# Performance work log

Measured on AMD Instinct MI355X. Metric: run time of the kernel, lower is better.

Reference implementation:

```python
import jax, jax.numpy as jnp
import numpy as np

# Static SMPL kinematic tree (24 joints)
PARENTS = [-1, 0, 0, 0, 1, 2, 3, 4, 5, 6, 7, 8, 9, 9, 9, 12, 13, 14, 16, 17, 18, 19, 20, 21]
NJ = 24      # num joints
FS = 6       # local_feature_size
NF = 7       # bone_dim (1) + FS


def _topo_order(parents):
    children = {i: [] for i in range(len(parents))}
    roots = []
    for i, p in enumerate(parents):
        (roots if p == -1 else children[p]).append(i)
    order = []
    queue = roots[:]
    while queue:
        c = queue.pop(0)
        order.append(c)
        queue.extend(sorted(children[c]))
    return order

TOPO = _topo_order(PARENTS)


def setup_inputs() -> dict:
    key = jax.random.key(0)
    ks = jax.random.split(key, 5)
    B = 524288
    x = jax.random.normal(ks[0], (B, NJ, 1), dtype=jnp.float32)
    s = 1.0 / np.sqrt(NF)
    # Stacked per-joint weights. For the root joint, the parent-feature rows of
    # W1 are multiplied by a zero virtual parent feature, which is exactly
    # equivalent to the original Linear(1, 7) root MLP.
    W1 = jax.random.uniform(ks[1], (NJ, NF, NF), jnp.float32, -s, s)
    b1 = jax.random.uniform(ks[2], (NJ, NF), jnp.float32, -s, s)
    W2 = jax.random.uniform(ks[3], (NJ, NF, FS), jnp.float32, -s, s)
    b2 = jax.random.uniform(ks[4], (NJ, FS), jnp.float32, -s, s)
    return {"x": x, "W1": W1, "b1": b1, "W2": W2, "b2": b2}


def reference(x, W1, b1, W2, b2):
    # x: [B, NJ, 1]; sequential propagation over the fixed kinematic tree.
    B = x.shape[0]
    feats = [None] * NJ
    zero_pf = jnp.zeros((B, FS), x.dtype)
    for i in TOPO:
        p = PARENTS[i]
        pf = zero_pf if p == -1 else feats[p]
        inp = jnp.concatenate([x[:, i, :], pf], axis=-1)  # [B, 7]
        h = jax.nn.relu(inp @ W1[i] + b1[i])               # [B, 7]
        feats[i] = jax.nn.relu(h @ W2[i] + b2[i])          # [B, 6]
    return jnp.concatenate(feats, axis=-1)                 # [B, 144]
```

## Files before the change

### kernel.cpp

```cpp
#include <hip/hip_runtime.h>

#define NJ 24
#define NF 7
#define FS 6
#define THREADS 256
#define CUNITS 12
#define PAD 13

typedef float v4f __attribute__((ext_vector_type(4)));

__device__ constexpr int kParents[NJ] = {-1, 0, 0, 0, 1, 2, 3, 4, 5, 6, 7, 8,
                                          9, 9, 9, 12, 13, 14, 16, 17, 18, 19, 20, 21};

#define JOINT(i)                                                              \
    {                                                                         \
        const int p_ = kParents[i];                                           \
        float inp_[NF];                                                       \
        inp_[0] = xr[i];                                                      \
        _Pragma("unroll")                                                     \
        for (int j = 0; j < FS; ++j)                                          \
            inp_[1 + j] = (p_ < 0) ? 0.0f : feats[(p_ < 0) ? 0 : p_][j];      \
        float h_[NF];                                                         \
        _Pragma("unroll")                                                     \
        for (int j = 0; j < NF; ++j) h_[j] = b1[(i) * NF + j];                \
        _Pragma("unroll")                                                     \
        for (int k = 0; k < NF; ++k) {                                        \
            const float a_ = inp_[k];                                         \
            _Pragma("unroll")                                                 \
            for (int j = 0; j < NF; ++j)                                      \
                h_[j] = fmaf(a_, W1[(i) * NF * NF + k * NF + j], h_[j]);      \
        }                                                                     \
        _Pragma("unroll")                                                     \
        for (int j = 0; j < NF; ++j) h_[j] = fmaxf(h_[j], 0.0f);              \
        float f_[FS];                                                         \
        _Pragma("unroll")                                                     \
        for (int j = 0; j < FS; ++j) f_[j] = b2[(i) * FS + j];                \
        _Pragma("unroll")                                                     \
        for (int k = 0; k < NF; ++k) {                                        \
            const float a_ = h_[k];                                           \
            _Pragma("unroll")                                                 \
            for (int j = 0; j < FS; ++j)                                      \
                f_[j] = fmaf(a_, W2[(i) * NF * FS + k * FS + j], f_[j]);      \
        }                                                                     \
        _Pragma("unroll")                                                     \
        for (int j = 0; j < FS; ++j) {                                        \
            f_[j] = fmaxf(f_[j], 0.0f);                                       \
            feats[i][j] = f_[j];                                              \
        }                                                                     \
        if ((i) & 1) {                                                        \
            const int pp_ = ((i) >> 1) & 3;                                   \
            v4f* st_ = myStage + pp_ * 3;                                     \
            st_[0] = (v4f){feats[(i) - 1][0], feats[(i) - 1][1],              \
                           feats[(i) - 1][2], feats[(i) - 1][3]};             \
            st_[1] = (v4f){feats[(i) - 1][4], feats[(i) - 1][5],              \
                           f_[0], f_[1]};                                     \
            st_[2] = (v4f){f_[2], f_[3], f_[4], f_[5]};                       \
        }                                                                     \
    }

#define FLUSH(C)                                                              \
    {                                                                         \
        _Pragma("unroll")                                                     \
        for (int j = 0; j < CUNITS; ++j) {                                    \
            const int G = j * 64 + lane;                                      \
            const int s = G / CUNITS;                                         \
            const int q = G - s * CUNITS;                                     \
            fr[j] = sm[wid][s * PAD + q];                                     \
        }                                                                     \
        _Pragma("unroll")                                                     \
        for (int j = 0; j < CUNITS; ++j) {                                    \
            v4f* dst_ = reinterpret_cast<v4f*>(                               \
                reinterpret_cast<char*>(obase) + voff[j] + (C) * 192);        \
            __builtin_nontemporal_store(fr[j], dst_);                         \
        }                                                                     \
    }

#define KEEP12(A)                                                             \
    asm volatile("" :: "v"(A[0]), "v"(A[1]), "v"(A[2]), "v"(A[3]),            \
                 "v"(A[4]), "v"(A[5]), "v"(A[6]), "v"(A[7]),                  \
                 "v"(A[8]), "v"(A[9]), "v"(A[10]), "v"(A[11]));

__global__ __launch_bounds__(THREADS, 3) void se1d_kernel(
    const float* __restrict__ x,
    const float* __restrict__ W1,
    const float* __restrict__ b1,
    const float* __restrict__ W2,
    const float* __restrict__ b2,
    float* __restrict__ out, int B)
{
    __shared__ v4f sm[THREADS / 64][64 * PAD];

    const int t    = threadIdx.x;
    const int lane = t & 63;
    const int wid  = __builtin_amdgcn_readfirstlane(threadIdx.x >> 6);
    const int b    = blockIdx.x * THREADS + t;
    const int wb   = blockIdx.x * THREADS + wid * 64;

    v4f* const myStage = &sm[wid][lane * PAD];
    v4f* const obase = reinterpret_cast<v4f*>(out) + (size_t)wb * 36;

    int voff[CUNITS];
    #pragma unroll
    for (int j = 0; j < CUNITS; ++j) {
        const int G = j * 64 + lane;
        const int s = G / CUNITS;
        const int q = G - s * CUNITS;
        voff[j] = (s * 36 + q) * 16;
    }

    float xr[NJ];
    {
        const v4f* xv = reinterpret_cast<const v4f*>(x + (size_t)b * NJ);
        #pragma unroll
        for (int c = 0; c < NJ / 4; ++c) {
            v4f v = __builtin_nontemporal_load(xv + c);
            xr[c * 4 + 0] = v.x; xr[c * 4 + 1] = v.y;
            xr[c * 4 + 2] = v.z; xr[c * 4 + 3] = v.w;
        }
    }

    float feats[NJ][FS];
    v4f fr[CUNITS];

    JOINT(0) JOINT(1) JOINT(2) JOINT(3) JOINT(4) JOINT(5) JOINT(6) JOINT(7)
    FLUSH(0);
    JOINT(8) JOINT(9) JOINT(10) JOINT(11)
    JOINT(12) JOINT(13) JOINT(14) JOINT(15)
    FLUSH(1);
    JOINT(16) JOINT(17) JOINT(18) JOINT(19)
    JOINT(20) JOINT(21) JOINT(22) JOINT(23)
    FLUSH(2);

    KEEP12(fr);
    (void)B;
}

extern "C" void kernel_launch(void* const* d_in, const int* in_sizes, int n_in,
                              void* d_out, int out_size, void* d_ws, size_t ws_size,
                              hipStream_t stream) {
    const float* x  = (const float*)d_in[0];
    const float* W1 = (const float*)d_in[1];
    const float* b1 = (const float*)d_in[2];
    const float* W2 = (const float*)d_in[3];
    const float* b2 = (const float*)d_in[4];
    float* out = (float*)d_out;
    const int B = in_sizes[0] / NJ;
    const int grid = B / THREADS;
    hipLaunchKernelGGL(se1d_kernel, dim3(grid), dim3(THREADS), 0, stream,
                       x, W1, b1, W2, b2, out, B);
}
```

Measured before the change: 92.71 us.

## Stage per-joint weights in LDS with padded vector layout, drop staging pad

Copies all W1/b1/W2/b2 into a padded shared-memory table at block start, so per-joint weights come from LDS as broadcast vector reads instead of scalar global loads. The output staging buffer loses its padding (stride 12 instead of 13), which may bring back LDS bank conflicts. Nontemporal loads and stores become plain ones, store offsets are recomputed inline instead of held in registers, and the occupancy hint drops from 3 to 2. The trade is an extra sync and a larger LDS footprint in exchange for cheaper weight fetches.

```diff
diff --git a/kernel.cpp b/kernel.cpp
--- a/kernel.cpp
+++ b/kernel.cpp
@@ -5,7 +5,7 @@
 #define FS 6
 #define THREADS 256
 #define CUNITS 12
-#define PAD 13
+#define JSTRIDE 128
 
 typedef float v4f __attribute__((ext_vector_type(4)));
 
@@ -21,33 +21,46 @@
         for (int j = 0; j < FS; ++j)                                          \
             inp_[1 + j] = (p_ < 0) ? 0.0f : feats[(p_ < 0) ? 0 : p_][j];      \
         float h_[NF];                                                         \
-        _Pragma("unroll")                                                     \
-        for (int j = 0; j < NF; ++j) h_[j] = b1[(i) * NF + j];                \
+        {                                                                     \
+            const v4f* bb = reinterpret_cast<const v4f*>(&sw[(i) * JSTRIDE + 56]); \
+            v4f u0 = bb[0], u1 = bb[1];                                       \
+            h_[0] = u0.x; h_[1] = u0.y; h_[2] = u0.z; h_[3] = u0.w;           \
+            h_[4] = u1.x; h_[5] = u1.y; h_[6] = u1.z;                         \
+        }                                                                     \
         _Pragma("unroll")                                                     \
         for (int k = 0; k < NF; ++k) {                                        \
             const float a_ = inp_[k];                                         \
-            _Pragma("unroll")                                                 \
-            for (int j = 0; j < NF; ++j)                                      \
-                h_[j] = fmaf(a_, W1[(i) * NF * NF + k * NF + j], h_[j]);      \
+            const v4f* wr = reinterpret_cast<const v4f*>(&sw[(i) * JSTRIDE + k * 8]); \
+            v4f w0 = wr[0], w1 = wr[1];                                       \
+            h_[0] = fmaf(a_, w0.x, h_[0]); h_[1] = fmaf(a_, w0.y, h_[1]);     \
+            h_[2] = fmaf(a_, w0.z, h_[2]); h_[3] = fmaf(a_, w0.w, h_[3]);     \
+            h_[4] = fmaf(a_, w1.x, h_[4]); h_[5] = fmaf(a_, w1.y, h_[5]);     \
+            h_[6] = fmaf(a_, w1.z, h_[6]);                                    \
         }                                                                     \
         _Pragma("unroll")                                                     \
         for (int j = 0; j < NF; ++j) h_[j] = fmaxf(h_[j], 0.0f);              \
         float f_[FS];                                                         \
-        _Pragma("unroll")                                                     \
-        for (int j = 0; j < FS; ++j) f_[j] = b2[(i) * FS + j];                \
+        {                                                                     \
+            const v4f* bb = reinterpret_cast<const v4f*>(&sw[(i) * JSTRIDE + 120]); \
+            v4f u0 = bb[0], u1 = bb[1];                                       \
+            f_[0] = u0.x; f_[1] = u0.y; f_[2] = u0.z; f_[3] = u0.w;           \
+            f_[4] = u1.x; f_[5] = u1.y;                                       \
+        }                                                                     \
         _Pragma("unroll")                                                     \
         for (int k = 0; k < NF; ++k) {                                        \
             const float a_ = h_[k];                                           \
-            _Pragma("unroll")                                                 \
-            for (int j = 0; j < FS; ++j)                                      \
-                f_[j] = fmaf(a_, W2[(i) * NF * FS + k * FS + j], f_[j]);      \
+            const v4f* wr = reinterpret_cast<const v4f*>(&sw[(i) * JSTRIDE + 64 + k * 8]); \
+            v4f w0 = wr[0], w1 = wr[1];                                       \
+            f_[0] = fmaf(a_, w0.x, f_[0]); f_[1] = fmaf(a_, w0.y, f_[1]);     \
+            f_[2] = fmaf(a_, w0.z, f_[2]); f_[3] = fmaf(a_, w0.w, f_[3]);     \
+            f_[4] = fmaf(a_, w1.x, f_[4]); f_[5] = fmaf(a_, w1.y, f_[5]);     \
         }                                                                     \
         _Pragma("unroll")                                                     \
         for (int j = 0; j < FS; ++j) {                                        \
             f_[j] = fmaxf(f_[j], 0.0f);                                       \
             feats[i][j] = f_[j];                                              \
         }                                                                     \
-        if ((i) & 1) {                                                        \
+        if ((i) & 1) {  \
             const int pp_ = ((i) >> 1) & 3;                                   \
             v4f* st_ = myStage + pp_ * 3;                                     \
             st_[0] = (v4f){feats[(i) - 1][0], feats[(i) - 1][1],              \
@@ -65,13 +78,16 @@
             const int G = j * 64 + lane;                                      \
             const int s = G / CUNITS;                                         \
             const int q = G - s * CUNITS;                                     \
-            fr[j] = sm[wid][s * PAD + q];                                     \
+            fr[j] = sm[wid][s * CUNITS + q];                                  \
         }                                                                     \
         _Pragma("unroll")                                                     \
         for (int j = 0; j < CUNITS; ++j) {                                    \
-            v4f* dst_ = reinterpret_cast<v4f*>(                               \
-                reinterpret_cast<char*>(obase) + voff[j] + (C) * 192);        \
-            __builtin_nontemporal_store(fr[j], dst_);                         \
+            const int G = j * 64 + lane;                                      \
+            const int s = G / CUNITS;                                         \
+            const int q = G - s * CUNITS;                                     \
+            *reinterpret_cast<v4f*>(                                          \
+                reinterpret_cast<char*>(obase) +                              \
+                (s * 36 + q) * 16 + (C) * 192) = fr[j];                       \
         }                                                                     \
     }
 
@@ -80,7 +96,7 @@
                  "v"(A[4]), "v"(A[5]), "v"(A[6]), "v"(A[7]),                  \
                  "v"(A[8]), "v"(A[9]), "v"(A[10]), "v"(A[11]));
 
-__global__ __launch_bounds__(THREADS, 3) void se1d_kernel(
+__global__ __launch_bounds__(THREADS, 2) void se1d_kernel(
     const float* __restrict__ x,
     const float* __restrict__ W1,
     const float* __restrict__ b1,
@@ -88,7 +104,8 @@
     const float* __restrict__ b2,
     float* __restrict__ out, int B)
 {
-    __shared__ v4f sm[THREADS / 64][64 * PAD];
+    __shared__ float sw[NJ * JSTRIDE];
+    __shared__ v4f sm[THREADS / 64][64 * CUNITS];
 
     const int t    = threadIdx.x;
     const int lane = t & 63;
@@ -96,28 +113,40 @@
     const int b    = blockIdx.x * THREADS + t;
     const int wb   = blockIdx.x * THREADS + wid * 64;
 
-    v4f* const myStage = &sm[wid][lane * PAD];
+    for (int idx = t; idx < NJ * JSTRIDE; idx += THREADS) {
+        const int jnt = idx >> 7, r = idx & 127;
+        float v = 0.0f;
+        if (r < 56) {
+            const int k = r >> 3, j = r & 7;
+            if (j < NF) v = W1[jnt * NF * NF + k * NF + j];
+        } else if (r < 64) {
+            const int j = r - 56;
+            if (j < NF) v = b1[jnt * NF + j];
+        } else if (r < 120) {
+            const int k = (r - 64) >> 3, j = (r - 64) & 7;
+            if (j < FS) v = W2[jnt * NF * FS + k * FS + j];
+        } else {
+            const int j = r - 120;
+            if (j < FS) v = b2[jnt * FS + j];
+        }
+        sw[idx] = v;
+    }
+
+    v4f* const myStage = &sm[wid][lane * CUNITS];
     v4f* const obase = reinterpret_cast<v4f*>(out) + (size_t)wb * 36;
-
-    int voff[CUNITS];
-    #pragma unroll
-    for (int j = 0; j < CUNITS; ++j) {
-        const int G = j * 64 + lane;
-        const int s = G / CUNITS;
-        const int q = G - s * CUNITS;
-        voff[j] = (s * 36 + q) * 16;
-    }
 
     float xr[NJ];
     {
         const v4f* xv = reinterpret_cast<const v4f*>(x + (size_t)b * NJ);
         #pragma unroll
         for (int c = 0; c < NJ / 4; ++c) {
-            v4f v = __builtin_nontemporal_load(xv + c);
+            v4f v = xv[c];
             xr[c * 4 + 0] = v.x; xr[c * 4 + 1] = v.y;
             xr[c * 4 + 2] = v.z; xr[c * 4 + 3] = v.w;
         }
     }
+
+    __syncthreads();
 
     float feats[NJ][FS];
     v4f fr[CUNITS];
```

Result: slower. 111.1 us (+19.8%).

## Process four batch groups per block with software-prefetched input loads

Applied to the files above, without the earlier changes.

Each block now handles four consecutive 256-row groups in a loop. The next group's x is prefetched into registers while the current group computes, and the launch grid shrinks by four. The aim is to hide input load latency and amortize per-block setup such as the voff computation. Occupancy hint drops from 3 to 2 because the prefetch buffer raises register pressure, which could reduce latency hiding across waves.

```diff
diff --git a/kernel.cpp b/kernel.cpp
--- a/kernel.cpp
+++ b/kernel.cpp
@@ -6,6 +6,7 @@
 #define THREADS 256
 #define CUNITS 12
 #define PAD 13
+#define KGROUPS 4
 
 typedef float v4f __attribute__((ext_vector_type(4)));
 
@@ -58,7 +59,7 @@
         }                                                                     \
     }
 
-#define FLUSH(C)                                                              \
+#define FLUSH(CBYTES)                                                         \
     {                                                                         \
         _Pragma("unroll")                                                     \
         for (int j = 0; j < CUNITS; ++j) {                                    \
@@ -69,8 +70,7 @@
         }                                                                     \
         _Pragma("unroll")                                                     \
         for (int j = 0; j < CUNITS; ++j) {                                    \
-            v4f* dst_ = reinterpret_cast<v4f*>(                               \
-                reinterpret_cast<char*>(obase) + voff[j] + (C) * 192);        \
+            v4f* dst_ = reinterpret_cast<v4f*>(obase + voff[j] + (CBYTES));   \
             __builtin_nontemporal_store(fr[j], dst_);                         \
         }                                                                     \
     }
@@ -80,7 +80,16 @@
                  "v"(A[4]), "v"(A[5]), "v"(A[6]), "v"(A[7]),                  \
                  "v"(A[8]), "v"(A[9]), "v"(A[10]), "v"(A[11]));
 
-__global__ __launch_bounds__(THREADS, 3) void se1d_kernel(
+#define UNPACK_X()                                                            \
+    {                                                                         \
+        _Pragma("unroll")                                                     \
+        for (int c = 0; c < 6; ++c) {                                         \
+            xr[c * 4 + 0] = xp[c].x; xr[c * 4 + 1] = xp[c].y;                 \
+            xr[c * 4 + 2] = xp[c].z; xr[c * 4 + 3] = xp[c].w;                 \
+        }                                                                     \
+    }
+
+__global__ __launch_bounds__(THREADS, 2) void se1d_kernel(
     const float* __restrict__ x,
     const float* __restrict__ W1,
     const float* __restrict__ b1,
@@ -93,11 +102,10 @@
     const int t    = threadIdx.x;
     const int lane = t & 63;
     const int wid  = __builtin_amdgcn_readfirstlane(threadIdx.x >> 6);
-    const int b    = blockIdx.x * THREADS + t;
-    const int wb   = blockIdx.x * THREADS + wid * 64;
+    const int b0   = blockIdx.x * (THREADS * KGROUPS) + t;
+    const int wb0  = blockIdx.x * (THREADS * KGROUPS) + wid * 64;
 
     v4f* const myStage = &sm[wid][lane * PAD];
-    v4f* const obase = reinterpret_cast<v4f*>(out) + (size_t)wb * 36;
 
     int voff[CUNITS];
     #pragma unroll
@@ -108,28 +116,43 @@
         voff[j] = (s * 36 + q) * 16;
     }
 
+    const float* xptr = x + (size_t)b0 * NJ;
+    char* obase = reinterpret_cast<char*>(reinterpret_cast<v4f*>(out) +
+                                          (size_t)wb0 * 36);
+
+    float feats[NJ][FS];
     float xr[NJ];
+    v4f xp[6];
+    v4f fr[CUNITS];
+
     {
-        const v4f* xv = reinterpret_cast<const v4f*>(x + (size_t)b * NJ);
+        const v4f* xv = reinterpret_cast<const v4f*>(xptr);
         #pragma unroll
-        for (int c = 0; c < NJ / 4; ++c) {
-            v4f v = __builtin_nontemporal_load(xv + c);
-            xr[c * 4 + 0] = v.x; xr[c * 4 + 1] = v.y;
-            xr[c * 4 + 2] = v.z; xr[c * 4 + 3] = v.w;
-        }
+        for (int c = 0; c < 6; ++c) xp[c] = __builtin_nontemporal_load(xv + c);
     }
 
-    float feats[NJ][FS];
-    v4f fr[CUNITS];
+    #pragma unroll 1
+    for (int g = 0; g < KGROUPS; ++g) {
+        UNPACK_X();
+        if (g + 1 < KGROUPS) {
+            const v4f* xv = reinterpret_cast<const v4f*>(
+                xptr + (size_t)(g + 1) * THREADS * NJ);
+            #pragma unroll
+            for (int c = 0; c < 6; ++c)
+                xp[c] = __builtin_nontemporal_load(xv + c);
+        }
 
-    JOINT(0) JOINT(1) JOINT(2) JOINT(3) JOINT(4) JOINT(5) JOINT(6) JOINT(7)
-    FLUSH(0);
-    JOINT(8) JOINT(9) JOINT(10) JOINT(11)
-    JOINT(12) JOINT(13) JOINT(14) JOINT(15)
-    FLUSH(1);
-    JOINT(16) JOINT(17) JOINT(18) JOINT(19)
-    JOINT(20) JOINT(21) JOINT(22) JOINT(23)
-    FLUSH(2);
+        JOINT(0) JOINT(1) JOINT(2) JOINT(3) JOINT(4) JOINT(5) JOINT(6) JOINT(7)
+        FLUSH(0);
+        JOINT(8) JOINT(9) JOINT(10) JOINT(11)
+        JOINT(12) JOINT(13) JOINT(14) JOINT(15)
+        FLUSH(192);
+        JOINT(16) JOINT(17) JOINT(18) JOINT(19)
+        JOINT(20) JOINT(21) JOINT(22) JOINT(23)
+        FLUSH(384);
+
+        obase += (size_t)THREADS * 36 * 16;
+    }
 
     KEEP12(fr);
     (void)B;
@@ -145,7 +168,7 @@
     const float* b2 = (const float*)d_in[4];
     float* out = (float*)d_out;
     const int B = in_sizes[0] / NJ;
-    const int grid = B / THREADS;
+    const int grid = B / (THREADS * KGROUPS);
     hipLaunchKernelGGL(se1d_kernel, dim3(grid), dim3(THREADS), 0, stream,
                        x, W1, b1, W2, b2, out, B);
 }
```

Result: slower. 138.7 us (+49.6%).
